# Kernel tuning notes

Hardware: AMD Instinct MI355X
Metric: run time of the kernel (lower is better)

The kernel has to match this reference:

```python
import jax, jax.numpy as jnp
import numpy as np


def setup_inputs() -> dict:
    key = jax.random.key(0)
    kx, kq, kk, kv = jax.random.split(key, 4)
    B, S, F, D = 4, 4096, 512, 64
    x = jax.random.normal(kx, (B, S, F), dtype=jnp.float32)
    Wq = jax.random.normal(kq, (F, D), dtype=jnp.float32) * 0.05
    Wk = jax.random.normal(kk, (F, D), dtype=jnp.float32) * 0.05
    Wv = jax.random.normal(kv, (F, D), dtype=jnp.float32) * 0.05
    return {"x": x, "Wq": Wq, "Wk": Wk, "Wv": Wv}


def reference(x, Wq, Wk, Wv):
    # x: [B,S,F]; Wq/Wk/Wv: [F,D]
    q = jnp.einsum('bsf,fd->bsd', x, Wq)
    k = jnp.einsum('bsf,fd->bsd', x, Wk)
    v = jnp.einsum('bsf,fd->bsd', x, Wv)
    scale = 1.0 / jnp.sqrt(jnp.asarray(Wq.shape[-1], dtype=x.dtype))
    scores = jnp.einsum('bqd,bkd->bqk', q, k) * scale  # [B,S,S]
    weights = jax.nn.softmax(scores, axis=-1)
    return jnp.einsum('bqk,bkd->bqd', weights, v)
```

## Files before the change

### kernel.cpp

```cpp
#include <hip/hip_runtime.h>

constexpr int Bc = 4, Sc = 4096, Fc = 512, Dc = 64;
constexpr int KT = 32;
constexpr int NT = (Sc / 4) / KT;

typedef __attribute__((ext_vector_type(8)))  short  short8;
typedef __attribute__((ext_vector_type(4)))  float  float4v;
typedef __attribute__((ext_vector_type(16))) float  float16v;
typedef __attribute__((ext_vector_type(2)))  unsigned int uint2v;

__device__ inline unsigned short f2bf(float f) {
    union { float f; unsigned u; } v; v.f = f;
    unsigned r = v.u + 0x7FFF + ((v.u >> 16) & 1);
    return (unsigned short)(r >> 16);
}
__device__ inline unsigned pk2(float a, float b) {
    union { float f; unsigned u; } x, y; x.f = a; y.f = b;
    unsigned ra = x.u + 0x7FFF + ((x.u >> 16) & 1);
    unsigned rb = y.u + 0x7FFF + ((y.u >> 16) & 1);
    return (ra >> 16) | (rb & 0xFFFF0000u);
}
__device__ inline unsigned cvtpk2(float lo, float hi) {
    unsigned r;
    asm("v_cvt_pk_bf16_f32 %0, %1, %2" : "=v"(r) : "v"(lo), "v"(hi));
    return r;
}
__device__ inline float exp2fast(float x) {
#if defined(__has_builtin) && __has_builtin(__builtin_amdgcn_exp2f)
    return __builtin_amdgcn_exp2f(x);
#else
    return __expf(x * 0.69314718055994531f);
#endif
}

__device__ inline void swap32(unsigned& a, unsigned& b) {
#if defined(__has_builtin) && __has_builtin(__builtin_amdgcn_permlane32_swap)
    uint2v r = __builtin_amdgcn_permlane32_swap(a, b, false, false);
    a = r[0]; b = r[1];
#else
    unsigned ax = (unsigned)__shfl_xor((int)a, 32);
    unsigned bx = (unsigned)__shfl_xor((int)b, 32);
    int upper = (threadIdx.x & 32) != 0;
    unsigned na = upper ? bx : a;
    unsigned nb = upper ? b  : ax;
    a = na; b = nb;
#endif
}

__global__ __launch_bounds__(256) void prep_kernel(
    const float* __restrict__ Wq, const float* __restrict__ Wk,
    const float* __restrict__ Wv, unsigned short* __restrict__ Wf)
{
    int wi = blockIdx.x * 256 + threadIdx.x;
    int lane = wi & 63;
    int kc = (wi >> 6) & 15;
    int nt = wi >> 10;
    int lm = lane & 15, quad = lane >> 4;
    int n = nt * 16 + lm;
    const float* W = (n < 64) ? Wq : (n < 128) ? Wk : Wv;
    int nc = n & 63;
    float scale = (n < 64) ? 0.18033688011112042f : 1.0f;
    int kbase = kc * 32 + quad * 8;
    union { uint4 v; unsigned short s[8]; } tmp;
    #pragma unroll
    for (int j = 0; j < 8; ++j)
        tmp.s[j] = f2bf(W[(size_t)(kbase + j) * Dc + nc] * scale);
    *(uint4*)&Wf[(size_t)wi * 8] = tmp.v;
}

__global__ __launch_bounds__(256) void qkv_kernel(
    const float* __restrict__ x, const unsigned short* __restrict__ Wf,
    unsigned short* __restrict__ Qb, unsigned short* __restrict__ Kb,
    unsigned short* __restrict__ Vtb)
{
    __shared__ __align__(16) unsigned short Xs[2][16][72];
    __shared__ __align__(16) unsigned short Ot[16][200];
    const int t = threadIdx.x;
    const int lane = t & 63, w = t >> 6;
    const int lm = lane & 15, quad = lane >> 4;
    const int row0 = blockIdx.x * 16;
    const int sr = t >> 4, sc4 = (t & 15) * 4;

    float4 xv;
    auto load_x = [&](int k0) {
        xv = *(const float4*)&x[(size_t)(row0 + sr) * Fc + k0 + sc4];
    };
    load_x(0);

    float4v acc[3];
    #pragma unroll
    for (int n = 0; n < 3; ++n) acc[n] = float4v{0.f, 0.f, 0.f, 0.f};

    int buf = 0;
    #pragma unroll
    for (int k0 = 0; k0 < Fc; k0 += 64, buf ^= 1) {
        uint2 pk;
        pk.x = pk2(xv.x, xv.y); pk.y = pk2(xv.z, xv.w);
        *(uint2*)&Xs[buf][sr][sc4] = pk;
        __syncthreads();
        if (k0 + 64 < Fc) load_x(k0 + 64);

        short8 af[2];
        #pragma unroll
        for (int h = 0; h < 2; ++h)
            af[h] = *(const short8*)&Xs[buf][lm][h * 32 + quad * 8];

        #pragma unroll
        for (int n = 0; n < 3; ++n) {
            const int nt = 3 * w + n;
            #pragma unroll
            for (int h = 0; h < 2; ++h) {
                const int kchunk = (k0 >> 5) + h;
                short8 bf_ = *(const short8*)&Wf[(size_t)((nt * 16 + kchunk) * 64 + lane) * 8];
                acc[n] = __builtin_amdgcn_mfma_f32_16x16x32_bf16(af[h], bf_, acc[n], 0, 0, 0);
            }
        }
    }

    __syncthreads();
    #pragma unroll
    for (int n = 0; n < 3; ++n)
        #pragma unroll
        for (int r = 0; r < 4; ++r)
            Ot[quad * 4 + r][(3 * w + n) * 16 + lm] = f2bf(acc[n][r]);
    __syncthreads();

    {
        const int r2 = t >> 4, c2 = (t & 15) * 4;
        *(uint2*)&Qb[(size_t)(row0 + r2) * Dc + c2] = *(const uint2*)&Ot[r2][c2];
        *(uint2*)&Kb[(size_t)(row0 + r2) * Dc + c2] = *(const uint2*)&Ot[r2][64 + c2];
    }
    {
        const int d = t >> 2, s4 = (t & 3) * 4;
        union { uint2 v; unsigned short s[4]; } tmp;
        #pragma unroll
        for (int j = 0; j < 4; ++j) tmp.s[j] = Ot[s4 + j][128 + d];
        const int bb = row0 >> 12, s0r = row0 & (Sc - 1);
        *(uint2*)&Vtb[((size_t)bb * Dc + d) * Sc + s0r + s4] = tmp.v;
    }
}

__global__ __launch_bounds__(256) void attn_kernel(
    const unsigned short* __restrict__ Qb, const unsigned short* __restrict__ Kb,
    const unsigned short* __restrict__ Vtb,
    float* __restrict__ out)
{
    __shared__ __align__(16) char smem[65536];

    const int t = threadIdx.x;
    const int lane = t & 63, w = t >> 6;
    const int l31 = lane & 31, lh = lane >> 5;

    const int orig = blockIdx.x;
    const int swz = (orig & 7) * 64 + (orig >> 3);
    const int b = swz >> 7;
    const int q0 = (swz & 127) * 32;
    const size_t qkbase = (size_t)b * Sc * Dc;
    const size_t vbase  = (size_t)b * Dc * Sc;
    const int kw0 = w * (Sc / 4);

    short8 qf[4];
    #pragma unroll
    for (int c = 0; c < 4; ++c)
        qf[c] = *(const short8*)&Qb[qkbase + (size_t)(q0 + l31) * Dc + c * 16 + lh * 8];

    float16v O0, O1;
    #pragma unroll
    for (int r = 0; r < 16; ++r) { O0[r] = 0.f; O1[r] = 0.f; }
    float lA = 0.f, lB = 0.f;

    char* const slice = smem + w * 16384;
    const int sk8 = (lane & 7) ^ ((lane >> 3) & 7);
    const int sv4 = (lane & 3) ^ ((lane >> 3) & 3);

    auto stage = [&](int p, int k0) {
        char* kb = slice + p * 8192;
        char* vb = kb + 4096;
        #pragma unroll
        for (int j = 0; j < 4; ++j) {
            const int krow = j * 8 + (lane >> 3);
            const unsigned short* gk = Kb + qkbase + (size_t)(k0 + krow) * Dc + sk8 * 8;
            __builtin_amdgcn_global_load_lds(
                (const __attribute__((address_space(1))) void*)gk,
                (__attribute__((address_space(3))) void*)(kb + j * 1024), 16, 0, 0);
            const int vrow = j * 16 + (lane >> 2);
            const unsigned short* gv = Vtb + vbase + (size_t)vrow * Sc + k0 + sv4 * 8;
            __builtin_amdgcn_global_load_lds(
                (const __attribute__((address_space(1))) void*)gv,
                (__attribute__((address_space(3))) void*)(vb + j * 1024), 16, 0, 0);
        }
    };

    auto rdK = [&](const char* kb, int row, int cc) -> short8 {
        return *(const short8*)(kb + row * 128 + ((cc ^ (row & 7)) * 16));
    };
    auto rdV = [&](const char* vb, int row, int cc) -> short8 {
        return *(const short8*)(vb + row * 64 + ((cc ^ ((row >> 1) & 3)) * 16));
    };

    auto mk_pb = [&](const float16v& s, int g) -> short8 {
        unsigned X0 = cvtpk2(s[8 * g + 0], s[8 * g + 1]);
        unsigned X1 = cvtpk2(s[8 * g + 2], s[8 * g + 3]);
        unsigned Y0 = cvtpk2(s[8 * g + 4], s[8 * g + 5]);
        unsigned Y1 = cvtpk2(s[8 * g + 6], s[8 * g + 7]);
        swap32(X0, Y0);
        swap32(X1, Y1);
        union { unsigned u[4]; short8 s8; } r;
        r.u[0] = X0; r.u[1] = X1; r.u[2] = Y0; r.u[3] = Y1;
        return r.s8;
    };

    stage(0, kw0);

    int p = 0;
    for (int kt = 0; kt < NT; ++kt, p ^= 1) {
        if (kt + 1 < NT) {
            stage(p ^ 1, kw0 + (kt + 1) * KT);
            asm volatile("s_waitcnt vmcnt(8)" ::: "memory");
        } else {
            asm volatile("s_waitcnt vmcnt(0)" ::: "memory");
        }
        __builtin_amdgcn_sched_barrier(0);
        const char* kb = slice + p * 8192;
        const char* vb = kb + 4096;

        float16v s;
        #pragma unroll
        for (int r = 0; r < 16; ++r) s[r] = 0.f;
        __builtin_amdgcn_s_setprio(1);
        #pragma unroll
        for (int c = 0; c < 4; ++c) {
            short8 a = rdK(kb, l31, 2 * c + lh);
            s = __builtin_amdgcn_mfma_f32_32x32x16_bf16(a, qf[c], s, 0, 0, 0);
        }
        __builtin_amdgcn_s_setprio(0);

        #pragma unroll
        for (int r = 0; r < 16; ++r) {
            float pe = exp2fast(s[r]); s[r] = pe;
            if (r < 8) lA += pe; else lB += pe;
        }

        short8 pb0 = mk_pb(s, 0);
        short8 pb1 = mk_pb(s, 1);

        __builtin_amdgcn_s_setprio(1);
        #pragma unroll
        for (int c = 0; c < 2; ++c) {
            short8 pb  = c ? pb1 : pb0;
            short8 va0 = rdV(vb, l31,      2 * c + lh);
            short8 va1 = rdV(vb, 32 + l31, 2 * c + lh);
            O0 = __builtin_amdgcn_mfma_f32_32x32x16_bf16(va0, pb, O0, 0, 0, 0);
            O1 = __builtin_amdgcn_mfma_f32_32x32x16_bf16(va1, pb, O1, 0, 0, 0);
        }
        __builtin_amdgcn_s_setprio(0);
    }

    float l_i = lA + lB;
    l_i += __shfl_xor(l_i, 32);

    float* Of = (float*)slice;
    #pragma unroll
    for (int r = 0; r < 16; ++r) {
        int d0 = (r & 3) + 8 * (r >> 2) + 4 * lh;
        Of[l31 * 68 + d0]      = O0[r];
        Of[l31 * 68 + 32 + d0] = O1[r];
    }
    float* lw = (float*)(slice + 8704);
    if (lane < 32) lw[l31] = l_i;

    __syncthreads();

    {
        const int q = t >> 3, d8 = (t & 7) * 8;
        float acc8[8];
        #pragma unroll
        for (int j = 0; j < 8; ++j) acc8[j] = 0.f;
        float L = 0.f;
        #pragma unroll
        for (int w2 = 0; w2 < 4; ++w2) {
            const float* OfW = (const float*)(smem + w2 * 16384);
            const float* lwW = (const float*)(smem + w2 * 16384 + 8704);
            L += lwW[q];
            #pragma unroll
            for (int j = 0; j < 8; ++j) acc8[j] += OfW[q * 68 + d8 + j];
        }
        float inv = 1.f / L;
        float4 o0, o1;
        o0.x = acc8[0] * inv; o0.y = acc8[1] * inv; o0.z = acc8[2] * inv; o0.w = acc8[3] * inv;
        o1.x = acc8[4] * inv; o1.y = acc8[5] * inv; o1.z = acc8[6] * inv; o1.w = acc8[7] * inv;
        float* op = out + ((size_t)b * Sc + q0 + q) * Dc + d8;
        *(float4*)op = o0;
        *(float4*)(op + 4) = o1;
    }
}

extern "C" void kernel_launch(void* const* d_in, const int* in_sizes, int n_in,
                              void* d_out, int out_size, void* d_ws, size_t ws_size,
                              hipStream_t stream) {
    const float* x  = (const float*)d_in[0];
    const float* Wq = (const float*)d_in[1];
    const float* Wk = (const float*)d_in[2];
    const float* Wv = (const float*)d_in[3];
    float* out = (float*)d_out;

    char* p = (char*)d_ws;
    unsigned short* Wf  = (unsigned short*)p;  p += (size_t)192 * Fc * 2;
    unsigned short* Qb  = (unsigned short*)p;  p += (size_t)Bc * Sc * Dc * 2;
    unsigned short* Kb  = (unsigned short*)p;  p += (size_t)Bc * Sc * Dc * 2;
    unsigned short* Vtb = (unsigned short*)p;

    prep_kernel<<<48, 256, 0, stream>>>(Wq, Wk, Wv, Wf);
    qkv_kernel<<<Bc * Sc / 16, 256, 0, stream>>>(x, Wf, Qb, Kb, Vtb);
    attn_kernel<<<dim3(Sc / 32 * Bc), 256, 0, stream>>>(Qb, Kb, Vtb, out);
}
```

Before: 118.5 us.

## Load V fragments directly from global into registers, halving per-wave LDS staging

V tiles are no longer staged through LDS with global_load_lds. Each lane now reads its MFMA A-operand fragments for V straight from global memory into registers at the start of each iteration. Only K stays double-buffered in LDS, so shared memory drops from 64KB to 36KB per block, which should allow more resident blocks per CU and removes the V LDS write and read traffic. The cost is narrow strided global reads (64 bytes per V row per tile) that depend on cache hits, and load latency that the compiler's own waits must cover inside the loop.

```diff
diff --git a/kernel.cpp b/kernel.cpp
--- a/kernel.cpp
+++ b/kernel.cpp
@@ -145,7 +145,7 @@
     const unsigned short* __restrict__ Vtb,
     float* __restrict__ out)
 {
-    __shared__ __align__(16) char smem[65536];
+    __shared__ __align__(16) char smem[36864];
 
     const int t = threadIdx.x;
     const int lane = t & 63, w = t >> 6;
@@ -169,13 +169,11 @@
     for (int r = 0; r < 16; ++r) { O0[r] = 0.f; O1[r] = 0.f; }
     float lA = 0.f, lB = 0.f;
 
-    char* const slice = smem + w * 16384;
+    char* const slice = smem + w * 9216;
     const int sk8 = (lane & 7) ^ ((lane >> 3) & 7);
-    const int sv4 = (lane & 3) ^ ((lane >> 3) & 3);
-
-    auto stage = [&](int p, int k0) {
-        char* kb = slice + p * 8192;
-        char* vb = kb + 4096;
+
+    auto stageK = [&](int p, int k0) {
+        char* kb = slice + p * 4096;
         #pragma unroll
         for (int j = 0; j < 4; ++j) {
             const int krow = j * 8 + (lane >> 3);
@@ -183,19 +181,11 @@
             __builtin_amdgcn_global_load_lds(
                 (const __attribute__((address_space(1))) void*)gk,
                 (__attribute__((address_space(3))) void*)(kb + j * 1024), 16, 0, 0);
-            const int vrow = j * 16 + (lane >> 2);
-            const unsigned short* gv = Vtb + vbase + (size_t)vrow * Sc + k0 + sv4 * 8;
-            __builtin_amdgcn_global_load_lds(
-                (const __attribute__((address_space(1))) void*)gv,
-                (__attribute__((address_space(3))) void*)(vb + j * 1024), 16, 0, 0);
         }
     };
 
     auto rdK = [&](const char* kb, int row, int cc) -> short8 {
         return *(const short8*)(kb + row * 128 + ((cc ^ (row & 7)) * 16));
-    };
-    auto rdV = [&](const char* vb, int row, int cc) -> short8 {
-        return *(const short8*)(vb + row * 64 + ((cc ^ ((row >> 1) & 3)) * 16));
     };
 
     auto mk_pb = [&](const float16v& s, int g) -> short8 {
@@ -210,19 +200,30 @@
         return r.s8;
     };
 
-    stage(0, kw0);
+    stageK(0, kw0);
 
     int p = 0;
     for (int kt = 0; kt < NT; ++kt, p ^= 1) {
+        const int kcur = kw0 + kt * KT;
+
+        short8 va[4];
+        {
+            const unsigned short* vp0 = Vtb + vbase + (size_t)l31 * Sc + kcur + lh * 8;
+            const unsigned short* vp1 = Vtb + vbase + (size_t)(32 + l31) * Sc + kcur + lh * 8;
+            va[0] = *(const short8*)vp0;
+            va[1] = *(const short8*)vp1;
+            va[2] = *(const short8*)(vp0 + 16);
+            va[3] = *(const short8*)(vp1 + 16);
+        }
+
         if (kt + 1 < NT) {
-            stage(p ^ 1, kw0 + (kt + 1) * KT);
+            stageK(p ^ 1, kcur + KT);
             asm volatile("s_waitcnt vmcnt(8)" ::: "memory");
         } else {
-            asm volatile("s_waitcnt vmcnt(0)" ::: "memory");
+            asm volatile("s_waitcnt vmcnt(4)" ::: "memory");
         }
         __builtin_amdgcn_sched_barrier(0);
-        const char* kb = slice + p * 8192;
-        const char* vb = kb + 4096;
+        const char* kb = slice + p * 4096;
 
         float16v s;
         #pragma unroll
@@ -245,14 +246,10 @@
         short8 pb1 = mk_pb(s, 1);
 
         __builtin_amdgcn_s_setprio(1);
-        #pragma unroll
-        for (int c = 0; c < 2; ++c) {
-            short8 pb  = c ? pb1 : pb0;
-            short8 va0 = rdV(vb, l31,      2 * c + lh);
-            short8 va1 = rdV(vb, 32 + l31, 2 * c + lh);
-            O0 = __builtin_amdgcn_mfma_f32_32x32x16_bf16(va0, pb, O0, 0, 0, 0);
-            O1 = __builtin_amdgcn_mfma_f32_32x32x16_bf16(va1, pb, O1, 0, 0, 0);
-        }
+        O0 = __builtin_amdgcn_mfma_f32_32x32x16_bf16(va[0], pb0, O0, 0, 0, 0);
+        O1 = __builtin_amdgcn_mfma_f32_32x32x16_bf16(va[1], pb0, O1, 0, 0, 0);
+        O0 = __builtin_amdgcn_mfma_f32_32x32x16_bf16(va[2], pb1, O0, 0, 0, 0);
+        O1 = __builtin_amdgcn_mfma_f32_32x32x16_bf16(va[3], pb1, O1, 0, 0, 0);
         __builtin_amdgcn_s_setprio(0);
     }
 
@@ -279,8 +276,8 @@
         float L = 0.f;
         #pragma unroll
         for (int w2 = 0; w2 < 4; ++w2) {
-            const float* OfW = (const float*)(smem + w2 * 16384);
-            const float* lwW = (const float*)(smem + w2 * 16384 + 8704);
+            const float* OfW = (const float*)(smem + w2 * 9216);
+            const float* lwW = (const float*)(smem + w2 * 9216 + 8704);
             L += lwW[q];
             #pragma unroll
             for (int j = 0; j < 8; ++j) acc8[j] += OfW[q * 68 + d8 + j];
```

After: 126.1 us. +6.4%, slower.
